# Kernel optimization log

Measured on AMD Instinct MI355X. Metric: run time of the kernel, lower is better.

Reference implementation:

```python
import jax, jax.numpy as jnp
import numpy as np

GAMMA1, GAMMA2, GAMMA3 = 4.0, 5.0, 10.0
BSIZE = 5
EPS = 1e-10


def _l2norm(x, axis):
    # torch F.normalize: x / max(||x||2, 1e-12)
    n = jnp.sqrt(jnp.sum(x * x, axis=axis, keepdims=True))
    return x / jnp.maximum(n, 1e-12)


def _block_score(v, e, M, HW):
    """calculate_matching_score for one block with uniform segment length.
    v: [B, R, D] flattened image regions (R = M*HW); e: [B, L, D] per-sample texts.
    Segments of the concatenated text are the B chunks of length L (lenAry cumulative).
    """
    B, R, D = v.shape
    L = e.shape[1]
    Tb = B * L
    ef = e.reshape(Tb, D)
    vf = v.reshape(B * R, D)
    s = vf @ ef.T                                        # [B*R, Tb]
    # per-text-segment softmax over text dim, then scale by gamma1
    s_nt = GAMMA1 * jax.nn.softmax(s.reshape(B * R, B, L), axis=-1)
    # attention over image regions
    alpha = jax.nn.softmax(s_nt.reshape(B, R, Tb), axis=1)
    v_tidal = jnp.einsum('brt,brd->btd', alpha, v)       # [B, Tb, D]
    logit = jnp.sum(_l2norm(v_tidal, 2) * _l2norm(ef, 1)[None], axis=2)  # [B, Tb]
    score1 = jnp.sum(jnp.exp(logit).reshape(B, B, L), axis=2)            # [B, B]
    lsm1 = jnp.log(score1 ** (1.0 / GAMMA2) + EPS)
    # beta path: softmax over all regions, exp, reduce over spatial cells
    s_nt2 = jax.nn.softmax(s.reshape(B, R, Tb), axis=1).reshape(B, M, HW, Tb)
    s_exp = jnp.exp(s_nt2)
    sd = jnp.sum(s_exp, axis=2)                          # [B, M, Tb]
    sd4 = sd.reshape(B, M, B, L)
    sd_seg = jnp.sum(sd4, axis=3, keepdims=True)         # per-segment denominators
    beta = sd4 / sd_seg                                  # [B, M, B, L] (= sum_hw s_exp / sd_rep)
    em = jnp.einsum('bmsl,sld->bmsd', beta, e)           # [B, M, B, D] (em_prime)
    # em is constant over the HW repeat axis, so the mean of dot products collapses:
    v_norm_sum = jnp.sum(_l2norm(v.reshape(B, M, HW, D), 3), axis=2)     # [B, M, D]
    logit2 = jnp.einsum('bmsd,bmd->bms', _l2norm(em, 3), v_norm_sum) / HW  # [B, M, B]
    score2 = jnp.sum(jnp.exp(logit2), axis=1) ** (1.0 / GAMMA2)          # [B, B]
    lsm2 = jnp.log(score2 + EPS)
    # beta decorrelation regularizer
    beta_f = beta.reshape(B, M, Tb)
    tmp = jnp.einsum('bmt,bnt->bmn', beta_f, beta_f)     # [B, M, M]
    off = tmp * (1.0 - jnp.eye(M, dtype=tmp.dtype))
    loss_reg = jnp.mean(jnp.sqrt(jnp.sum(off * off, axis=(1, 2))))
    lsm = GAMMA3 * (lsm1 + lsm2)
    d = jnp.diagonal(lsm)
    pdq = -jnp.sum(jnp.log(d / jnp.sum(lsm, axis=1) + EPS))
    pqd = -jnp.sum(jnp.log(d / jnp.sum(lsm, axis=0) + EPS))
    return (pdq + pqd) / B + loss_reg


def setup_inputs() -> dict:
    key = jax.random.key(0)
    k1, k2 = jax.random.split(key)
    B, M, D, H_r, H_w, L = 40, 8, 256, 16, 16, 15
    image = jax.random.normal(k1, (B, M, D, H_r, H_w), dtype=jnp.float32)
    text = jax.random.normal(k2, (B, L, D), dtype=jnp.float32)
    length_info = jnp.full((B,), L, dtype=jnp.int32)  # uniform lengths (max = 15)
    return {'image': image, 'text': text, 'length_info': length_info}


def reference(image, text, length_info):
    B, M, D, H_r, H_w = image.shape
    HW = H_r * H_w
    R = M * HW
    # (shuffle omitted for determinism; identity permutation)
    img = jnp.transpose(image, (0, 1, 3, 4, 2)).reshape(B, R, D)
    nblk = B // BSIZE
    v_blocks = img.reshape(nblk, BSIZE, R, D)
    e_blocks = text.reshape(nblk, BSIZE, text.shape[1], D)
    scores = jax.vmap(lambda v, e: _block_score(v, e, M, HW))(v_blocks, e_blocks)
    numBlcks = B // BSIZE + 1  # faithful to int(B/bsize)+1 in the source
    return jnp.sum(scores) / numBlcks
```

## Files before the change

### kernel.cpp

```cpp
#include <hip/hip_runtime.h>
#include <hip/hip_bf16.h>
#include <math.h>

#define NG 8
#define NB5 5
#define NM 8
#define NHW 256
#define NR 2048
#define ND 256
#define NL 15
#define NT 75
#define NGB 40

#define OFF_S    0
#define SZ_S     (NGB*NT*NR)
#define OFF_W    (OFF_S + SZ_S)
#define OFF_RMAX (OFF_W + SZ_S)
#define SZ_RST   (NGB*5*NR)
#define OFF_RSUM (OFF_RMAX + SZ_RST)
#define OFF_SD   (OFF_RSUM + SZ_RST)
#define SZ_SD    (NGB*NM*NT)
#define OFF_VNS  (OFF_SD + SZ_SD)
#define SZ_VNS   (NGB*NM*ND)
#define OFF_LG   (OFF_VNS + SZ_VNS)
#define SZ_LG    (NGB*NT)
#define OFF_LG2  (OFF_LG + SZ_LG)
#define SZ_LG2   (NGB*NM*5)
#define OFF_BETA (OFF_LG2 + SZ_LG2)
#define SZ_BETA  (NGB*NM*NT)
#define OFF_BLK  (OFF_BETA + SZ_BETA)

__device__ __forceinline__ float bredsum(float v, float* red) {
    int tid = threadIdx.x;
    red[tid] = v; __syncthreads();
    for (int s2 = 128; s2 > 0; s2 >>= 1) {
        if (tid < s2) red[tid] += red[tid + s2];
        __syncthreads();
    }
    float r = red[0]; __syncthreads();
    return r;
}

__global__ __launch_bounds__(256, 2) void k1_gemm_s(const float* __restrict__ image,
                                                    const float* __restrict__ text,
                                                    float* __restrict__ ws) {
    __shared__ __align__(16) float A[32][260];
    __shared__ __align__(16) float Et[32][52];
    float* Sg = ws + OFF_S;
    int blk = blockIdx.x;
    int th = blk >= 320 ? 1 : 0;
    int rest = blk - th * 320;
    int m = rest & 7, gb = rest >> 3;
    int g = gb / 5;
    int tb = th * 40;
    const float* cell = image + (size_t)(gb * 8 + m) * ND * NHW;
    int tid = threadIdx.x;
    int lane = tid & 63;
    int w = __builtin_amdgcn_readfirstlane(tid >> 6);
    int hw4 = lane * 4;
    int arow = tid >> 6;
    int acol = (tid & 63) * 4;
    int edd  = tid & 31;
    int etc0 = tid >> 5;
    float4 acc[10];
#pragma unroll
    for (int j = 0; j < 10; ++j) acc[j] = make_float4(0.f, 0.f, 0.f, 0.f);
    float4 p0, p1, p2, p3, p4, p5, p6, p7;
    float e0, e1, e2, e3, e4;
    const float* tbase = text + (size_t)g * 75 * 256;
#define K1_T(I) ((tb + etc0 + 8 * (I)) > 74 ? 74 : (tb + etc0 + 8 * (I)))
#define K1_LOAD(D0)                                                              \
    p0 = *(const float4*)&cell[(size_t)((D0) + arow +  0) * 256 + acol];         \
    p1 = *(const float4*)&cell[(size_t)((D0) + arow +  4) * 256 + acol];         \
    p2 = *(const float4*)&cell[(size_t)((D0) + arow +  8) * 256 + acol];         \
    p3 = *(const float4*)&cell[(size_t)((D0) + arow + 12) * 256 + acol];         \
    p4 = *(const float4*)&cell[(size_t)((D0) + arow + 16) * 256 + acol];         \
    p5 = *(const float4*)&cell[(size_t)((D0) + arow + 20) * 256 + acol];         \
    p6 = *(const float4*)&cell[(size_t)((D0) + arow + 24) * 256 + acol];         \
    p7 = *(const float4*)&cell[(size_t)((D0) + arow + 28) * 256 + acol];         \
    e0 = tbase[(size_t)K1_T(0) * 256 + (D0) + edd];                              \
    e1 = tbase[(size_t)K1_T(1) * 256 + (D0) + edd];                              \
    e2 = tbase[(size_t)K1_T(2) * 256 + (D0) + edd];                              \
    e3 = tbase[(size_t)K1_T(3) * 256 + (D0) + edd];                              \
    e4 = tbase[(size_t)K1_T(4) * 256 + (D0) + edd];
#define K1_ECOL(I) (((etc0 + 8 * (I)) / 10) * 12 + ((etc0 + 8 * (I)) % 10))
    K1_LOAD(0)
    for (int c = 0; c < 8; ++c) {
        __syncthreads();
        *(float4*)&A[arow +  0][acol] = p0;
        *(float4*)&A[arow +  4][acol] = p1;
        *(float4*)&A[arow +  8][acol] = p2;
        *(float4*)&A[arow + 12][acol] = p3;
        *(float4*)&A[arow + 16][acol] = p4;
        *(float4*)&A[arow + 20][acol] = p5;
        *(float4*)&A[arow + 24][acol] = p6;
        *(float4*)&A[arow + 28][acol] = p7;
        Et[edd][K1_ECOL(0)] = e0;
        Et[edd][K1_ECOL(1)] = e1;
        Et[edd][K1_ECOL(2)] = e2;
        Et[edd][K1_ECOL(3)] = e3;
        Et[edd][K1_ECOL(4)] = e4;
        __syncthreads();
        if (c < 7) { K1_LOAD((c + 1) * 32) }
        for (int dd = 0; dd < 32; ++dd) {
            float4 av = *(const float4*)&A[dd][hw4];
            float4 q0 = *(const float4*)&Et[dd][w * 12];
            float4 q1 = *(const float4*)&Et[dd][w * 12 + 4];
            float2 q2 = *(const float2*)&Et[dd][w * 12 + 8];
            float ev[10] = {q0.x, q0.y, q0.z, q0.w, q1.x, q1.y, q1.z, q1.w, q2.x, q2.y};
#pragma unroll
            for (int j = 0; j < 10; ++j) {
                acc[j].x += av.x * ev[j]; acc[j].y += av.y * ev[j];
                acc[j].z += av.z * ev[j]; acc[j].w += av.w * ev[j];
            }
        }
    }
#undef K1_LOAD
#undef K1_T
#undef K1_ECOL
#pragma unroll
    for (int j = 0; j < 10; ++j) {
        int t = tb + w * 10 + j;
        if (t < 75)
            *(float4*)&Sg[((size_t)gb * 75 + t) * 2048 + m * 256 + hw4] = acc[j];
    }
}

__global__ __launch_bounds__(256) void k2_rowstats(float* __restrict__ ws) {
    const float* Sg = ws + OFF_S;
    float* RMAX = ws + OFF_RMAX;
    float* RSUM = ws + OFF_RSUM;
    int blk = blockIdx.x;
    int m = blk & 7, gb = blk >> 3;
    int r = m * 256 + threadIdx.x;
    const float* base = Sg + (size_t)gb * 75 * 2048 + r;
    for (int seg = 0; seg < 5; ++seg) {
        float v[15]; float mx = -1e30f;
#pragma unroll
        for (int l = 0; l < 15; ++l) {
            v[l] = base[(size_t)(seg * 15 + l) * 2048];
            mx = fmaxf(mx, v[l]);
        }
        float sm = 0.f;
#pragma unroll
        for (int l = 0; l < 15; ++l) sm += __expf(v[l] - mx);
        RMAX[((size_t)gb * 5 + seg) * 2048 + r] = mx;
        RSUM[((size_t)gb * 5 + seg) * 2048 + r] = sm;
    }
}

__global__ __launch_bounds__(256) void k3_colstats(float* __restrict__ ws) {
    __shared__ float red[256];
    __shared__ float red8[8][256];
    const float* Sg = ws + OFF_S;
    const float* RMAX = ws + OFF_RMAX;
    const float* RSUM = ws + OFF_RSUM;
    float* W = ws + OFF_W;
    float* SD = ws + OFF_SD;
    int blk = blockIdx.x;
    int t = blk % 75, gb = blk / 75;
    int seg = t / 15;
    int tid = threadIdx.x;
    const float* col = Sg + ((size_t)gb * 75 + t) * 2048;
    const float* rmx = RMAX + ((size_t)gb * 5 + seg) * 2048;
    const float* rsm = RSUM + ((size_t)gb * 5 + seg) * 2048;
    float sv[8], ent[8];
    float lmax = -1e30f, lsnt = 0.f;
#pragma unroll
    for (int k = 0; k < 8; ++k) {
        int r = tid + 256 * k;
        float s = col[r];
        sv[k] = s;
        float snt = 4.f * __expf(s - rmx[r]) / rsm[r];
        float e = __expf(snt);
        ent[k] = e;
        lsnt += e;
        lmax = fmaxf(lmax, s);
    }
    red[tid] = lmax; __syncthreads();
    for (int s2 = 128; s2 > 0; s2 >>= 1) {
        if (tid < s2) red[tid] = fmaxf(red[tid], red[tid + s2]);
        __syncthreads();
    }
    float cmax = red[0]; __syncthreads();
    float pe[8]; float lse = 0.f;
#pragma unroll
    for (int k = 0; k < 8; ++k) { pe[k] = __expf(sv[k] - cmax); lse += pe[k]; }
    float csum = bredsum(lse, red);
    float csnt = bredsum(lsnt, red);
    float inv = 1.f / csnt;
#pragma unroll
    for (int k = 0; k < 8; ++k)
        W[((size_t)gb * 75 + t) * 2048 + tid + 256 * k] = ent[k] * inv;
    float icsum = 1.f / csum;
#pragma unroll
    for (int k = 0; k < 8; ++k) red8[k][tid] = __expf(pe[k] * icsum);
    __syncthreads();
    for (int s2 = 128; s2 > 0; s2 >>= 1) {
        if (tid < s2) {
#pragma unroll
            for (int k2 = 0; k2 < 8; ++k2) red8[k2][tid] += red8[k2][tid + s2];
        }
        __syncthreads();
    }
    if (tid < 8) SD[((size_t)gb * 8 + tid) * 75 + t] = red8[tid][0];
}

__global__ __launch_bounds__(256, 2) void k4_vtidal(const float* __restrict__ image,
                                                    float* __restrict__ ws) {
    __shared__ __align__(16) float V[32][260];
    __shared__ __align__(16) float WtT[32][52];
    const float* W = ws + OFF_W;
    float* VTP = ws + OFF_S;
    int blk = blockIdx.x;
    int th = blk >= 320 ? 1 : 0;
    int rest = blk - th * 320;
    int m = rest & 7, gb = rest >> 3;
    int tb = th * 40;
    const float* cell = image + (size_t)(gb * 8 + m) * ND * NHW;
    int tid = threadIdx.x;
    int lane = tid & 63;
    int w = __builtin_amdgcn_readfirstlane(tid >> 6);
    int d4 = lane * 4;
    int rr4  = (tid & 7) * 4;
    int drow = tid >> 3;
    int wrr  = tid & 31;
    int wtc0 = tid >> 5;
    float4 acc[10];
#pragma unroll
    for (int j = 0; j < 10; ++j) acc[j] = make_float4(0.f, 0.f, 0.f, 0.f);
    const float* wb = W + (size_t)gb * 75 * 2048 + m * 256;
    float4 p0, p1, p2, p3, p4, p5, p6, p7;
    float w0, w1, w2, w3, w4;
#define K4_T(I) ((tb + wtc0 + 8 * (I)) > 74 ? 74 : (tb + wtc0 + 8 * (I)))
#define K4_LOAD(RC)                                                               \
    p0 = *(const float4*)&cell[(size_t)(drow +   0) * 256 + (RC) * 32 + rr4];     \
    p1 = *(const float4*)&cell[(size_t)(drow +  32) * 256 + (RC) * 32 + rr4];     \
    p2 = *(const float4*)&cell[(size_t)(drow +  64) * 256 + (RC) * 32 + rr4];     \
    p3 = *(const float4*)&cell[(size_t)(drow +  96) * 256 + (RC) * 32 + rr4];     \
    p4 = *(const float4*)&cell[(size_t)(drow + 128) * 256 + (RC) * 32 + rr4];     \
    p5 = *(const float4*)&cell[(size_t)(drow + 160) * 256 + (RC) * 32 + rr4];     \
    p6 = *(const float4*)&cell[(size_t)(drow + 192) * 256 + (RC) * 32 + rr4];     \
    p7 = *(const float4*)&cell[(size_t)(drow + 224) * 256 + (RC) * 32 + rr4];     \
    w0 = wb[(size_t)K4_T(0) * 2048 + (RC) * 32 + wrr];                            \
    w1 = wb[(size_t)K4_T(1) * 2048 + (RC) * 32 + wrr];                            \
    w2 = wb[(size_t)K4_T(2) * 2048 + (RC) * 32 + wrr];                            \
    w3 = wb[(size_t)K4_T(3) * 2048 + (RC) * 32 + wrr];                            \
    w4 = wb[(size_t)K4_T(4) * 2048 + (RC) * 32 + wrr];
#define K4_WCOL(I) (((wtc0 + 8 * (I)) / 10) * 12 + ((wtc0 + 8 * (I)) % 10))
#define K4_VST(P, DOFF)                                                           \
    V[rr4 + 0][drow + (DOFF)] = (P).x;                                            \
    V[rr4 + 1][drow + (DOFF)] = (P).y;                                            \
    V[rr4 + 2][drow + (DOFF)] = (P).z;                                            \
    V[rr4 + 3][drow + (DOFF)] = (P).w;
    K4_LOAD(0)
    for (int rc = 0; rc < 8; ++rc) {
        __syncthreads();
        K4_VST(p0,   0) K4_VST(p1,  32) K4_VST(p2,  64) K4_VST(p3,  96)
        K4_VST(p4, 128) K4_VST(p5, 160) K4_VST(p6, 192) K4_VST(p7, 224)
        WtT[wrr][K4_WCOL(0)] = w0;
        WtT[wrr][K4_WCOL(1)] = w1;
        WtT[wrr][K4_WCOL(2)] = w2;
        WtT[wrr][K4_WCOL(3)] = w3;
        WtT[wrr][K4_WCOL(4)] = w4;
        __syncthreads();
        if (rc < 7) { K4_LOAD(rc + 1) }
        for (int rr = 0; rr < 32; ++rr) {
            float4 vv = *(const float4*)&V[rr][d4];
            float4 q0 = *(const float4*)&WtT[rr][w * 12];
            float4 q1 = *(const float4*)&WtT[rr][w * 12 + 4];
            float2 q2 = *(const float2*)&WtT[rr][w * 12 + 8];
            float wv[10] = {q0.x, q0.y, q0.z, q0.w, q1.x, q1.y, q1.z, q1.w, q2.x, q2.y};
#pragma unroll
            for (int j = 0; j < 10; ++j) {
                acc[j].x += vv.x * wv[j]; acc[j].y += vv.y * wv[j];
                acc[j].z += vv.z * wv[j]; acc[j].w += vv.w * wv[j];
            }
        }
    }
#undef K4_LOAD
#undef K4_T
#undef K4_WCOL
#undef K4_VST
#pragma unroll
    for (int j = 0; j < 10; ++j) {
        int t = tb + w * 10 + j;
        if (t < 75)
            *(float4*)&VTP[((size_t)(gb * 8 + m) * 75 + t) * 256 + d4] = acc[j];
    }
}

__global__ __launch_bounds__(256) void k5_logit(const float* __restrict__ text,
                                                float* __restrict__ ws) {
    __shared__ float red[256];
    const float* VTP = ws + OFF_S;
    float* LG = ws + OFF_LG;
    int blk = blockIdx.x;
    int t = blk % 75, gb = blk / 75, g = gb / 5;
    int tid = threadIdx.x;
    float vt = 0.f;
#pragma unroll
    for (int m = 0; m < 8; ++m)
        vt += VTP[((size_t)(gb * 8 + m) * 75 + t) * 256 + tid];
    int seg = t / 15, l = t % 15;
    float ev = text[((size_t)(g * 5 + seg) * 15 + l) * 256 + tid];
    float nvt = bredsum(vt * vt, red);
    float nev = bredsum(ev * ev, red);
    float dot = bredsum(vt * ev, red);
    if (tid == 0)
        LG[gb * 75 + t] = dot / (fmaxf(sqrtf(nvt), 1e-12f) * fmaxf(sqrtf(nev), 1e-12f));
}

__global__ __launch_bounds__(256) void k6_vns(const float* __restrict__ image,
                                              float* __restrict__ ws) {
    __shared__ float A[32][257];
    __shared__ float rn[256];
    __shared__ float ps[256];
    float* VNS = ws + OFF_VNS;
    int blk = blockIdx.x;
    int m = blk & 7, gb = blk >> 3;
    const float* cell = image + (size_t)(gb * 8 + m) * ND * NHW;
    int tid = threadIdx.x;
    float nsq = 0.f;
    for (int d = 0; d < 256; ++d) {
        float v = cell[d * 256 + tid];
        nsq += v * v;
    }
    rn[tid] = 1.f / fmaxf(sqrtf(nsq), 1e-12f);
    int d_loc = tid & 31, sub = tid >> 5;
    for (int d0 = 0; d0 < 256; d0 += 32) {
        __syncthreads();
#pragma unroll
        for (int i = 0; i < 32; ++i) A[i][tid] = cell[(d0 + i) * 256 + tid];
        __syncthreads();
        float partial = 0.f;
#pragma unroll
        for (int k = 0; k < 32; ++k) {
            int hw = sub + 8 * k;
            partial += A[d_loc][hw] * rn[hw];
        }
        ps[tid] = partial; __syncthreads();
        if (tid < 128) ps[tid] += ps[tid + 128];
        __syncthreads();
        if (tid < 64) ps[tid] += ps[tid + 64];
        __syncthreads();
        if (tid < 32)
            VNS[((size_t)gb * 8 + m) * 256 + d0 + tid] = ps[tid] + ps[tid + 32];
    }
}

__global__ __launch_bounds__(256) void k7_em(const float* __restrict__ text,
                                             float* __restrict__ ws) {
    __shared__ float red[256];
    __shared__ float sdv[75];
    __shared__ float segs[5];
    __shared__ float betas[5][15];
    const float* SD = ws + OFF_SD;
    const float* VNS = ws + OFF_VNS;
    float* BETA = ws + OFF_BETA;
    float* LG2 = ws + OFF_LG2;
    int blk = blockIdx.x;
    int m = blk & 7, gb = blk >> 3, g = gb / 5;
    int tid = threadIdx.x;
    if (tid < 75) sdv[tid] = SD[((size_t)gb * 8 + m) * 75 + tid];
    __syncthreads();
    if (tid < 5) {
        float s = 0.f;
        for (int l = 0; l < 15; ++l) s += sdv[tid * 15 + l];
        segs[tid] = s;
    }
    __syncthreads();
    if (tid < 75) {
        float b = sdv[tid] / segs[tid / 15];
        betas[tid / 15][tid % 15] = b;
        BETA[((size_t)gb * 8 + m) * 75 + tid] = b;
    }
    __syncthreads();
    float vns = VNS[((size_t)gb * 8 + m) * 256 + tid];
    for (int s = 0; s < 5; ++s) {
        float em = 0.f;
#pragma unroll
        for (int l = 0; l < 15; ++l)
            em += betas[s][l] * text[((size_t)(g * 5 + s) * 15 + l) * 256 + tid];
        float nem = bredsum(em * em, red);
        float dot = bredsum(em * vns, red);
        if (tid == 0)
            LG2[((size_t)gb * 8 + m) * 5 + s] =
                dot / fmaxf(sqrtf(nem), 1e-12f) * (1.f / 256.f);
        __syncthreads();
    }
}

__global__ __launch_bounds__(256) void k8_final(float* __restrict__ ws) {
    __shared__ float lsm[5][5];
    __shared__ float offsq[5][64];
    __shared__ float regs[5];
    const float* LG = ws + OFF_LG;
    const float* LG2 = ws + OFF_LG2;
    const float* BETA = ws + OFF_BETA;
    float* BLK = ws + OFF_BLK;
    int g = blockIdx.x;
    int tid = threadIdx.x;
    if (tid < 25) {
        int b = tid / 5, s = tid % 5;
        int gb = g * 5 + b;
        float s1 = 0.f;
        for (int l = 0; l < 15; ++l) s1 += expf(LG[gb * 75 + s * 15 + l]);
        float s2 = 0.f;
        for (int mm = 0; mm < 8; ++mm) s2 += expf(LG2[((size_t)gb * 8 + mm) * 5 + s]);
        float l1 = logf(powf(s1, 0.2f) + 1e-10f);
        float l2 = logf(powf(s2, 0.2f) + 1e-10f);
        lsm[b][s] = 10.f * (l1 + l2);
    }
    for (int p = tid; p < 320; p += 256) {
        int b = p >> 6, mn = p & 63, mm = mn >> 3, nn = mn & 7;
        int gb = g * 5 + b;
        const float* bm = BETA + ((size_t)gb * 8 + mm) * 75;
        const float* bn = BETA + ((size_t)gb * 8 + nn) * 75;
        float acc = 0.f;
        for (int t2 = 0; t2 < 75; ++t2) acc += bm[t2] * bn[t2];
        offsq[b][mn] = (mm == nn) ? 0.f : acc * acc;
    }
    __syncthreads();
    if (tid < 5) {
        float s = 0.f;
        for (int i = 0; i < 64; ++i) s += offsq[tid][i];
        regs[tid] = sqrtf(s);
    }
    __syncthreads();
    if (tid == 0) {
        float loss_reg = 0.f;
        for (int b = 0; b < 5; ++b) loss_reg += regs[b];
        loss_reg *= 0.2f;
        float pdq = 0.f, pqd = 0.f;
        for (int i = 0; i < 5; ++i) {
            float rsum = 0.f, csum = 0.f;
            for (int j = 0; j < 5; ++j) { rsum += lsm[i][j]; csum += lsm[j][i]; }
            float di = lsm[i][i];
            pdq += -logf(di / rsum + 1e-10f);
            pqd += -logf(di / csum + 1e-10f);
        }
        BLK[g] = (pdq + pqd) * 0.2f + loss_reg;
    }
}

__global__ void k9_out(const float* __restrict__ ws, float* __restrict__ out) {
    if (threadIdx.x == 0) {
        float s = 0.f;
        for (int g2 = 0; g2 < 8; ++g2) s += ws[OFF_BLK + g2];
        out[0] = s / 9.f;
    }
}

extern "C" void kernel_launch(void* const* d_in, const int* in_sizes, int n_in,
                              void* d_out, int out_size, void* d_ws, size_t ws_size,
                              hipStream_t stream) {
    const float* image = (const float*)d_in[0];
    const float* text  = (const float*)d_in[1];
    float* ws = (float*)d_ws;
    float* out = (float*)d_out;
    hipLaunchKernelGGL(k1_gemm_s,   dim3(640),  dim3(256), 0, stream, image, text, ws);
    hipLaunchKernelGGL(k2_rowstats, dim3(320),  dim3(256), 0, stream, ws);
    hipLaunchKernelGGL(k3_colstats, dim3(3000), dim3(256), 0, stream, ws);
    hipLaunchKernelGGL(k4_vtidal,   dim3(640),  dim3(256), 0, stream, image, ws);
    hipLaunchKernelGGL(k5_logit,    dim3(3000), dim3(256), 0, stream, text, ws);
    hipLaunchKernelGGL(k6_vns,      dim3(320),  dim3(256), 0, stream, image, ws);
    hipLaunchKernelGGL(k7_em,       dim3(320),  dim3(256), 0, stream, text, ws);
    hipLaunchKernelGGL(k8_final,    dim3(8),    dim3(256), 0, stream, ws);
    hipLaunchKernelGGL(k9_out,      dim3(1),    dim3(64),  0, stream, ws, out);
}
```

Baseline: 298.8 us.

## Drop LDS staging in score GEMM and stream operands directly from global

The shared-memory tiling of the image-text GEMM kernel is removed. Each wave now loads image float4 rows from global memory with register double-buffering, and reads text vectors with wave-uniform addresses, so the block barriers go away. The aim is to cut LDS traffic and synchronisation. In exchange, each of the four waves re-reads the same image tile from cache, which adds redundant global/L2 traffic.

```diff
diff --git a/kernel.cpp b/kernel.cpp
--- a/kernel.cpp
+++ b/kernel.cpp
@@ -44,8 +44,6 @@
 __global__ __launch_bounds__(256, 2) void k1_gemm_s(const float* __restrict__ image,
                                                     const float* __restrict__ text,
                                                     float* __restrict__ ws) {
-    __shared__ __align__(16) float A[32][260];
-    __shared__ __align__(16) float Et[32][52];
     float* Sg = ws + OFF_S;
     int blk = blockIdx.x;
     int th = blk >= 320 ? 1 : 0;
@@ -54,73 +52,57 @@
     int g = gb / 5;
     int tb = th * 40;
     const float* cell = image + (size_t)(gb * 8 + m) * ND * NHW;
+    const float* tbase = text + (size_t)g * 75 * 256;
     int tid = threadIdx.x;
     int lane = tid & 63;
     int w = __builtin_amdgcn_readfirstlane(tid >> 6);
     int hw4 = lane * 4;
-    int arow = tid >> 6;
-    int acol = (tid & 63) * 4;
-    int edd  = tid & 31;
-    int etc0 = tid >> 5;
+    int t0 = tb + w * 10;
+    int tt[10];
+#pragma unroll
+    for (int j = 0; j < 10; ++j) { int t = t0 + j; tt[j] = t > 74 ? 74 : t; }
     float4 acc[10];
 #pragma unroll
     for (int j = 0; j < 10; ++j) acc[j] = make_float4(0.f, 0.f, 0.f, 0.f);
-    float4 p0, p1, p2, p3, p4, p5, p6, p7;
-    float e0, e1, e2, e3, e4;
-    const float* tbase = text + (size_t)g * 75 * 256;
-#define K1_T(I) ((tb + etc0 + 8 * (I)) > 74 ? 74 : (tb + etc0 + 8 * (I)))
-#define K1_LOAD(D0)                                                              \
-    p0 = *(const float4*)&cell[(size_t)((D0) + arow +  0) * 256 + acol];         \
-    p1 = *(const float4*)&cell[(size_t)((D0) + arow +  4) * 256 + acol];         \
-    p2 = *(const float4*)&cell[(size_t)((D0) + arow +  8) * 256 + acol];         \
-    p3 = *(const float4*)&cell[(size_t)((D0) + arow + 12) * 256 + acol];         \
-    p4 = *(const float4*)&cell[(size_t)((D0) + arow + 16) * 256 + acol];         \
-    p5 = *(const float4*)&cell[(size_t)((D0) + arow + 20) * 256 + acol];         \
-    p6 = *(const float4*)&cell[(size_t)((D0) + arow + 24) * 256 + acol];         \
-    p7 = *(const float4*)&cell[(size_t)((D0) + arow + 28) * 256 + acol];         \
-    e0 = tbase[(size_t)K1_T(0) * 256 + (D0) + edd];                              \
-    e1 = tbase[(size_t)K1_T(1) * 256 + (D0) + edd];                              \
-    e2 = tbase[(size_t)K1_T(2) * 256 + (D0) + edd];                              \
-    e3 = tbase[(size_t)K1_T(3) * 256 + (D0) + edd];                              \
-    e4 = tbase[(size_t)K1_T(4) * 256 + (D0) + edd];
-#define K1_ECOL(I) (((etc0 + 8 * (I)) / 10) * 12 + ((etc0 + 8 * (I)) % 10))
-    K1_LOAD(0)
-    for (int c = 0; c < 8; ++c) {
-        __syncthreads();
-        *(float4*)&A[arow +  0][acol] = p0;
-        *(float4*)&A[arow +  4][acol] = p1;
-        *(float4*)&A[arow +  8][acol] = p2;
-        *(float4*)&A[arow + 12][acol] = p3;
-        *(float4*)&A[arow + 16][acol] = p4;
-        *(float4*)&A[arow + 20][acol] = p5;
-        *(float4*)&A[arow + 24][acol] = p6;
-        *(float4*)&A[arow + 28][acol] = p7;
-        Et[edd][K1_ECOL(0)] = e0;
-        Et[edd][K1_ECOL(1)] = e1;
-        Et[edd][K1_ECOL(2)] = e2;
-        Et[edd][K1_ECOL(3)] = e3;
-        Et[edd][K1_ECOL(4)] = e4;
-        __syncthreads();
-        if (c < 7) { K1_LOAD((c + 1) * 32) }
-        for (int dd = 0; dd < 32; ++dd) {
-            float4 av = *(const float4*)&A[dd][hw4];
-            float4 q0 = *(const float4*)&Et[dd][w * 12];
-            float4 q1 = *(const float4*)&Et[dd][w * 12 + 4];
-            float2 q2 = *(const float2*)&Et[dd][w * 12 + 8];
-            float ev[10] = {q0.x, q0.y, q0.z, q0.w, q1.x, q1.y, q1.z, q1.w, q2.x, q2.y};
-#pragma unroll
-            for (int j = 0; j < 10; ++j) {
-                acc[j].x += av.x * ev[j]; acc[j].y += av.y * ev[j];
-                acc[j].z += av.z * ev[j]; acc[j].w += av.w * ev[j];
-            }
-        }
-    }
-#undef K1_LOAD
-#undef K1_T
-#undef K1_ECOL
+#define K1_LD(DD) (*(const float4*)&cell[(size_t)(DD) * 256 + hw4])
+    float4 a0 = K1_LD(0), a1 = K1_LD(1), a2 = K1_LD(2), a3 = K1_LD(3);
+    for (int c = 0; c < 64; ++c) {
+        int dd = c * 4;
+        float4 n0, n1, n2, n3;
+        if (c < 63) {
+            n0 = K1_LD(dd + 4); n1 = K1_LD(dd + 5);
+            n2 = K1_LD(dd + 6); n3 = K1_LD(dd + 7);
+        }
+        float4 e4[10];
+#pragma unroll
+        for (int j = 0; j < 10; ++j)
+            e4[j] = *(const float4*)&tbase[(size_t)tt[j] * 256 + dd];
+#pragma unroll
+        for (int j = 0; j < 10; ++j) {
+            acc[j].x += a0.x * e4[j].x; acc[j].y += a0.y * e4[j].x;
+            acc[j].z += a0.z * e4[j].x; acc[j].w += a0.w * e4[j].x;
+        }
+#pragma unroll
+        for (int j = 0; j < 10; ++j) {
+            acc[j].x += a1.x * e4[j].y; acc[j].y += a1.y * e4[j].y;
+            acc[j].z += a1.z * e4[j].y; acc[j].w += a1.w * e4[j].y;
+        }
+#pragma unroll
+        for (int j = 0; j < 10; ++j) {
+            acc[j].x += a2.x * e4[j].z; acc[j].y += a2.y * e4[j].z;
+            acc[j].z += a2.z * e4[j].z; acc[j].w += a2.w * e4[j].z;
+        }
+#pragma unroll
+        for (int j = 0; j < 10; ++j) {
+            acc[j].x += a3.x * e4[j].w; acc[j].y += a3.y * e4[j].w;
+            acc[j].z += a3.z * e4[j].w; acc[j].w += a3.w * e4[j].w;
+        }
+        if (c < 63) { a0 = n0; a1 = n1; a2 = n2; a3 = n3; }
+    }
+#undef K1_LD
 #pragma unroll
     for (int j = 0; j < 10; ++j) {
-        int t = tb + w * 10 + j;
+        int t = t0 + j;
         if (t < 75)
             *(float4*)&Sg[((size_t)gb * 75 + t) * 2048 + m * 256 + hw4] = acc[j];
     }
```

After: 300.4 us. No clear change (+0.5%).
